# Optimization experiments

Hardware: AMD Instinct MI355X
Metric: run time of the kernel (lower is better)

The kernel has to match this reference:

```python
import jax, jax.numpy as jnp
import numpy as np

L, B, N, C, H = 6, 4, 512, 512, 8
D = C // H          # head_dim = 64
MLP = 4 * C         # mlp_ratio = 4.0
EPS = 1e-6


def setup_inputs() -> dict:
    key = jax.random.key(0)
    ks = jax.random.split(key, 12)
    p = lambda k, sh: jax.random.normal(k, sh, dtype=jnp.float32) * 0.02
    return {
        "x": jax.random.normal(ks[0], (B, N, C), dtype=jnp.float32),
        "time_emb": jax.random.normal(ks[1], (B, C), dtype=jnp.float32),
        "pair_emb": jax.random.normal(ks[2], (B, H, N, N), dtype=jnp.float32) * 0.1,
        "is_padded_mask": jnp.zeros((B, 1, 1, N), dtype=bool),
        # per-block stacked params (leading dim = L blocks)
        "wq": p(ks[3], (L, C, C)),
        "wk": p(ks[4], (L, C, C)),
        "wv": p(ks[5], (L, C, C)),
        "wo": p(ks[6], (L, C, C)),
        "bo": jnp.zeros((L, C), dtype=jnp.float32),
        "w1": p(ks[7], (L, C, MLP)),
        "b1": jnp.zeros((L, MLP), dtype=jnp.float32),
        "w2": p(ks[8], (L, MLP, C)),
        "b2": jnp.zeros((L, C), dtype=jnp.float32),
        "wada": p(ks[9], (L, C, 6 * C)),
        "bada": jnp.zeros((L, 6 * C), dtype=jnp.float32),
    }


def _ln(x):
    # LayerNorm without affine, eps=1e-6 (torch elementwise_affine=False)
    mu = jnp.mean(x, axis=-1, keepdims=True)
    var = jnp.mean(jnp.square(x - mu), axis=-1, keepdims=True)
    return (x - mu) * jax.lax.rsqrt(var + EPS)


def _modulate(x, shift, scale):
    return x * (1.0 + scale[:, None, :]) + shift[:, None, :]


def reference(x, time_emb, pair_emb, is_padded_mask,
              wq, wk, wv, wo, bo, w1, b1, w2, b2, wada, bada):
    scale = D ** -0.5
    t_act = jax.nn.silu(time_emb)  # shared SiLU input to adaLN of each block
    for i in range(L):
        ada = t_act @ wada[i] + bada[i]  # (B, 6C)
        sh_msa, sc_msa, g_msa, sh_mlp, sc_mlp, g_mlp = jnp.split(ada, 6, axis=1)
        # fill_attn_mask: masked_fill padded key positions with -inf
        pair = jnp.where(is_padded_mask, -jnp.inf, pair_emb)  # (B,H,N,N)
        mx = _modulate(_ln(x), sh_msa, sc_msa)  # (B,N,C)
        q = (mx @ wq[i]).reshape(B, N, H, D)
        k = (mx @ wk[i]).reshape(B, N, H, D)
        v = (mx @ wv[i]).reshape(B, N, H, D)
        qk = jnp.einsum('bnhd,bshd->bhns', q, k) * scale  # (B,H,N,N)
        attn = jax.nn.softmax(qk + pair, axis=-1)
        o = jnp.einsum('bhns,bshd->bnhd', attn, v).reshape(B, N, C)
        o = o @ wo[i] + bo[i]
        x = x + g_msa[:, None, :] * o
        pair_emb = pair + qk  # residual on pair embedding
        h = _modulate(_ln(x), sh_mlp, sc_mlp)
        h = jax.nn.gelu(h @ w1[i] + b1[i], approximate=True) @ w2[i] + b2[i]
        x = x + g_mlp[:, None, :] * h
    return x, pair_emb
```

## Files before the change

kernel.cpp:

```cpp
#include <hip/hip_runtime.h>
#include <hip/hip_bf16.h>

#define LNUM 6
#define BB 4
#define NSEQ 512
#define CDIM 512
#define HNUM 8
#define DHEAD 64
#define MLPD 2048
#define MROWS (BB*NSEQ)

typedef __hip_bfloat16 bf16;
typedef __attribute__((ext_vector_type(4))) float f32x4;
typedef __attribute__((ext_vector_type(8))) short bf16x8;

__device__ __forceinline__ void gld_lds16(const bf16* g, bf16* l) {
  __builtin_amdgcn_global_load_lds((const __attribute__((address_space(1))) void*)g,
                                   (__attribute__((address_space(3))) void*)l, 16, 0, 0);
}

__device__ __forceinline__ float gelu_tanh(float t) {
  float u = 0.7978845608028654f * (t + 0.044715f * t * t * t);
  u = fminf(fmaxf(u, -15.f), 15.f);
  float e = __expf(2.f * u);
  return 0.5f * t * (1.f + (e - 1.f) / (e + 1.f));
}

enum { EP_BF16 = 0, EP_RESID = 2, EP_GELU = 3, EP_QKV = 4 };

template<int BM, int BN, int MODE>
__global__ __launch_bounds__(256) void gemm_nt(
    const bf16* __restrict__ A, int lda,
    const bf16* __restrict__ Bt, int ldb,
    int K, int zdiv,
    long sA1, long sA2, long sB1, long sB2, long sO1, long sO2,
    bf16* __restrict__ obf, int ldo,
    const float* __restrict__ bias,
    const float* __restrict__ ada, int gate_off,
    float* __restrict__ xres,
    bf16* __restrict__ vtout)
{
  constexpr int FM = BM / 32, FN = BN / 32;
  __shared__ bf16 lA[2 * BM * 64];
  __shared__ bf16 lB[2 * BN * 64];
  const int tid = threadIdx.x;
  const int wid = tid >> 6, lane = tid & 63;
  const int z = blockIdx.z;
  const long z1 = z / zdiv, z2 = z % zdiv;
  A  += z1 * sA1 + z2 * sA2;
  Bt += z1 * sB1 + z2 * sB2;
  const long obase = z1 * sO1 + z2 * sO2;
  const int m0 = blockIdx.x * BM;
  const int n0 = blockIdx.y * BN;
  const int wm = wid >> 1, wn = wid & 1;
  const int srow = tid >> 3, scl = tid & 7;

  f32x4 zero = {0.f, 0.f, 0.f, 0.f};
  f32x4 acc[FM][FN];
#pragma unroll
  for (int i = 0; i < FM; i++)
#pragma unroll
    for (int j = 0; j < FN; j++) acc[i][j] = zero;

  auto stage = [&](int buf, int kt) {
#pragma unroll
    for (int p = 0; p < BM / 32; p++) {
      const int rr = (p << 5) + srow;
      const int gk = (scl ^ (rr & 7)) << 3;
      gld_lds16(A + (size_t)(m0 + rr) * lda + (kt << 6) + gk,
                lA + buf * (BM * 64) + (p << 11) + (wid << 9));
    }
#pragma unroll
    for (int p = 0; p < BN / 32; p++) {
      const int rr = (p << 5) + srow;
      const int gk = (scl ^ (rr & 7)) << 3;
      gld_lds16(Bt + (size_t)(n0 + rr) * ldb + (kt << 6) + gk,
                lB + buf * (BN * 64) + (p << 11) + (wid << 9));
    }
  };

  const int rlo = lane & 15, kq = lane >> 4;
  auto compute = [&](int buf) {
#pragma unroll
    for (int kk = 0; kk < 2; kk++) {
      bf16x8 af[FM], bg[FN];
#pragma unroll
      for (int i = 0; i < FM; i++) {
        const int ra = wm * (BM / 2) + (i << 4) + rlo;
        af[i] = *(const bf16x8*)(lA + buf * (BM * 64) + (ra << 6) +
                                 ((((kk << 2) + kq) ^ (ra & 7)) << 3));
      }
#pragma unroll
      for (int j = 0; j < FN; j++) {
        const int rb2 = wn * (BN / 2) + (j << 4) + rlo;
        bg[j] = *(const bf16x8*)(lB + buf * (BN * 64) + (rb2 << 6) +
                                 ((((kk << 2) + kq) ^ (rb2 & 7)) << 3));
      }
#pragma unroll
      for (int i = 0; i < FM; i++)
#pragma unroll
        for (int j = 0; j < FN; j++)
          acc[i][j] = __builtin_amdgcn_mfma_f32_16x16x32_bf16(af[i], bg[j], acc[i][j], 0, 0, 0);
    }
  };

  const int NT = K >> 6;
  stage(0, 0);
  for (int t = 0; t < NT - 1; t++) {
    stage((t + 1) & 1, t + 1);
    if constexpr ((BM + BN) / 32 == 4)      asm volatile("s_waitcnt vmcnt(4)" ::: "memory");
    else if constexpr ((BM + BN) / 32 == 6) asm volatile("s_waitcnt vmcnt(6)" ::: "memory");
    else                                    asm volatile("s_waitcnt vmcnt(8)" ::: "memory");
    __builtin_amdgcn_s_barrier();
    asm volatile("" ::: "memory");
    compute(t & 1);
    asm volatile("" ::: "memory");
    __builtin_amdgcn_s_barrier();
  }
  asm volatile("s_waitcnt vmcnt(0)" ::: "memory");
  __builtin_amdgcn_s_barrier();
  asm volatile("" ::: "memory");
  compute((NT - 1) & 1);

  const int cl = lane & 15, rb = (lane >> 4) << 2;
#pragma unroll
  for (int i = 0; i < FM; i++) {
#pragma unroll
    for (int j = 0; j < FN; j++) {
      const int gc = n0 + wn * (BN / 2) + (j << 4) + cl;
#pragma unroll
      for (int r = 0; r < 4; r++) {
        const int gr = m0 + wm * (BM / 2) + (i << 4) + rb + r;
        float v = acc[i][j][r];
        if (MODE == EP_BF16) {
          obf[obase + (size_t)gr * ldo + gc] = __float2bfloat16(v);
        } else if (MODE == EP_QKV) {
          if (gc < 2 * CDIM) {
            obf[obase + (size_t)gr * ldo + gc] = __float2bfloat16(v);
          } else {
            const int b = gr >> 9, n = gr & 511, hd = gc - 2 * CDIM;
            vtout[((size_t)((b << 3) + (hd >> 6)) * 64 + (hd & 63)) * 512 + n] = __float2bfloat16(v);
          }
        } else if (MODE == EP_RESID) {
          const int b = gr >> 9;
          float t2 = v + bias[gc];
          xres[(size_t)gr * CDIM + gc] += ada[b * (6 * CDIM) + gate_off + gc] * t2;
        } else {
          float t2 = v + bias[gc];
          obf[obase + (size_t)gr * ldo + gc] = __float2bfloat16(gelu_tanh(t2));
        }
      }
    }
  }
}

__global__ __launch_bounds__(256) void attn_fused(
    const bf16* __restrict__ qkv, const bf16* __restrict__ vt,
    const float* __restrict__ pair_in, float* __restrict__ pair_out,
    const unsigned char* __restrict__ mask,
    bf16* __restrict__ obuf, float scale)
{
  __shared__ bf16 lQ[64 * 64];
  __shared__ bf16 lK[2][64 * 64];
  __shared__ bf16 lV[2][64 * 64];
  __shared__ bf16 lP[64 * 64];
  const int tid = threadIdx.x, wid = tid >> 6;
  const int lane = tid & 63;
  const int z = blockIdx.z, b = z >> 3, h = z & 7;
  const int m0 = blockIdx.x * 64;
  const int srow = tid >> 3, scl = tid & 7;
  const bf16* Aq = qkv + (size_t)b * NSEQ * 1536 + h * 64;
  const bf16* Bk = Aq + CDIM;
  const bf16* Bv = vt + (size_t)z * DHEAD * NSEQ;
  const size_t pz = (size_t)z * NSEQ * NSEQ;
  const int rlo = lane & 15, kq = lane >> 4, cl = rlo;

#pragma unroll
  for (int r = 0; r < 2; r++) {
    const int rr = (r << 5) + srow;
    const int gk = (scl ^ (rr & 7)) << 3;
    gld_lds16(Aq + (size_t)(m0 + rr) * 1536 + gk, lQ + (r << 11) + (wid << 9));
    gld_lds16(Bk + (size_t)rr * 1536 + gk, lK[0] + (r << 11) + (wid << 9));
    gld_lds16(Bv + (size_t)rr * NSEQ + gk, lV[0] + (r << 11) + (wid << 9));
  }

  float m_run[4], l_run[4];
  f32x4 oacc[4];
  f32x4 zero = {0.f, 0.f, 0.f, 0.f};
#pragma unroll
  for (int r = 0; r < 4; r++) { m_run[r] = -INFINITY; l_run[r] = 0.f; }
#pragma unroll
  for (int j = 0; j < 4; j++) oacc[j] = zero;
  bf16x8 afq[2];

  float prA[4][4]; bool mkA[4];
  float prB[4][4]; bool mkB[4];
#pragma unroll
  for (int j = 0; j < 4; j++) {
#pragma unroll
    for (int r = 0; r < 4; r++)
      prA[j][r] = pair_in[pz + (size_t)(m0 + (wid << 4) + (kq << 2) + r) * NSEQ + ((j << 4) + cl)];
    mkA[j] = mask[b * NSEQ + (j << 4) + cl] != 0;
  }

  for (int ct = 0; ct < 8; ct++) {
    const int cur = ct & 1;
    asm volatile("s_waitcnt vmcnt(0)" ::: "memory");
    __builtin_amdgcn_s_barrier();
    asm volatile("" ::: "memory");

    if (ct == 0) {
#pragma unroll
      for (int kk = 0; kk < 2; kk++) {
        const int ra = (wid << 4) + rlo;
        afq[kk] = *(const bf16x8*)(lQ + (ra << 6) + ((((kk << 2) + kq) ^ (ra & 7)) << 3));
      }
    }

    if (ct < 7) {
#pragma unroll
      for (int r = 0; r < 2; r++) {
        const int rr = (r << 5) + srow;
        const int gk = (scl ^ (rr & 7)) << 3;
        gld_lds16(Bk + (size_t)((ct + 1) * 64 + rr) * 1536 + gk,
                  lK[cur ^ 1] + (r << 11) + (wid << 9));
        gld_lds16(Bv + (size_t)rr * NSEQ + (ct + 1) * 64 + gk,
                  lV[cur ^ 1] + (r << 11) + (wid << 9));
      }
#pragma unroll
      for (int j = 0; j < 4; j++) {
#pragma unroll
        for (int r = 0; r < 4; r++)
          prB[j][r] = pair_in[pz + (size_t)(m0 + (wid << 4) + (kq << 2) + r) * NSEQ +
                              ((ct + 1) * 64 + (j << 4) + cl)];
        mkB[j] = mask[b * NSEQ + (ct + 1) * 64 + (j << 4) + cl] != 0;
      }
    }

    f32x4 s[4];
#pragma unroll
    for (int j = 0; j < 4; j++) s[j] = zero;
#pragma unroll
    for (int kk = 0; kk < 2; kk++)
#pragma unroll
      for (int j = 0; j < 4; j++) {
        const int rk = (j << 4) + rlo;
        bf16x8 bk = *(const bf16x8*)(lK[cur] + (rk << 6) + ((((kk << 2) + kq) ^ (rk & 7)) << 3));
        s[j] = __builtin_amdgcn_mfma_f32_16x16x32_bf16(afq[kk], bk, s[j], 0, 0, 0);
      }

    float p[4][4];
#pragma unroll
    for (int r = 0; r < 4; r++) {
      const size_t prow = pz + (size_t)(m0 + (wid << 4) + (kq << 2) + r) * NSEQ + ct * 64;
      float sf[4];
#pragma unroll
      for (int j = 0; j < 4; j++) {
        float pp = mkA[j] ? -INFINITY : prA[j][r];
        sf[j] = s[j][r] * scale + pp;
        pair_out[prow + (j << 4) + cl] = sf[j];
      }
      float tm = fmaxf(fmaxf(sf[0], sf[1]), fmaxf(sf[2], sf[3]));
#pragma unroll
      for (int o = 1; o < 16; o <<= 1) tm = fmaxf(tm, __shfl_xor(tm, o));
      const float mnew = fmaxf(m_run[r], tm);
      const float fr = __expf(m_run[r] - mnew);
      float rs = 0.f;
#pragma unroll
      for (int j = 0; j < 4; j++) { p[j][r] = __expf(sf[j] - mnew); rs += p[j][r]; }
#pragma unroll
      for (int o = 1; o < 16; o <<= 1) rs += __shfl_xor(rs, o);
      l_run[r] = l_run[r] * fr + rs;
      m_run[r] = mnew;
#pragma unroll
      for (int j = 0; j < 4; j++) oacc[j][r] *= fr;
    }

#pragma unroll
    for (int j = 0; j < 4; j++)
#pragma unroll
      for (int r = 0; r < 4; r++) {
        const int row = (wid << 4) + (kq << 2) + r;
        const int col = (j << 4) + cl;
        lP[(row << 6) + (((col >> 3) ^ (row & 7)) << 3) + (col & 7)] = __float2bfloat16(p[j][r]);
      }
    asm volatile("s_waitcnt lgkmcnt(0)" ::: "memory");
    __builtin_amdgcn_sched_barrier(0);

#pragma unroll
    for (int kk = 0; kk < 2; kk++) {
      const int ra = (wid << 4) + rlo;
      bf16x8 ap = *(const bf16x8*)(lP + (ra << 6) + ((((kk << 2) + kq) ^ (ra & 7)) << 3));
#pragma unroll
      for (int j = 0; j < 4; j++) {
        const int rd = (j << 4) + rlo;
        bf16x8 bv = *(const bf16x8*)(lV[cur] + (rd << 6) + ((((kk << 2) + kq) ^ (rd & 7)) << 3));
        oacc[j] = __builtin_amdgcn_mfma_f32_16x16x32_bf16(ap, bv, oacc[j], 0, 0, 0);
      }
    }

    if (ct < 7) {
#pragma unroll
      for (int j = 0; j < 4; j++) {
#pragma unroll
        for (int r = 0; r < 4; r++) prA[j][r] = prB[j][r];
        mkA[j] = mkB[j];
      }
    }
  }

#pragma unroll
  for (int j = 0; j < 4; j++)
#pragma unroll
    for (int r = 0; r < 4; r++) {
      const int gr = m0 + (wid << 4) + (kq << 2) + r;
      const int gc = h * 64 + (j << 4) + cl;
      obuf[((size_t)b * NSEQ + gr) * CDIM + gc] = __float2bfloat16(oacc[j][r] / l_run[r]);
    }
}

__global__ __launch_bounds__(256) void ln_mod(const float* __restrict__ x,
                                              const float* __restrict__ ada,
                                              int sh_off, int sc_off,
                                              bf16* __restrict__ out)
{
  const int row = blockIdx.x;
  const int b = row >> 9;
  const float* xr = x + (size_t)row * CDIM;
  const int t = threadIdx.x;
  float2 v = ((const float2*)xr)[t];
  float s = v.x + v.y;
  float ss = v.x * v.x + v.y * v.y;
#pragma unroll
  for (int o = 32; o > 0; o >>= 1) { s += __shfl_down(s, o); ss += __shfl_down(ss, o); }
  __shared__ float red[8];
  __shared__ float mv[2];
  const int w = t >> 6, ln = t & 63;
  if (ln == 0) { red[w] = s; red[4 + w] = ss; }
  __syncthreads();
  if (t == 0) {
    float S = red[0] + red[1] + red[2] + red[3];
    float SS = red[4] + red[5] + red[6] + red[7];
    float mu = S * (1.0f / CDIM);
    float var = SS * (1.0f / CDIM) - mu * mu;
    mv[0] = mu; mv[1] = rsqrtf(var + 1e-6f);
  }
  __syncthreads();
  const float mu = mv[0], rs = mv[1];
  const float* adab = ada + b * (6 * CDIM);
  const int c = t * 2;
  float o0 = (v.x - mu) * rs * (1.0f + adab[sc_off + c])     + adab[sh_off + c];
  float o1 = (v.y - mu) * rs * (1.0f + adab[sc_off + c + 1]) + adab[sh_off + c + 1];
  out[(size_t)row * CDIM + c]     = __float2bfloat16(o0);
  out[(size_t)row * CDIM + c + 1] = __float2bfloat16(o1);
}

__global__ __launch_bounds__(256) void ada_part(const float* __restrict__ te,
                                                const float* __restrict__ wada,
                                                float* __restrict__ partial)
{
  __shared__ float ta[4][64];
  const int layer = blockIdx.z, kc = blockIdx.y;
  const int t = threadIdx.x;
  {
    const int b = t >> 6, kk = t & 63;
    float xx = te[b * CDIM + kc * 64 + kk];
    ta[b][kk] = xx / (1.f + __expf(-xx));
  }
  __syncthreads();
  const int col = blockIdx.x * 512 + t * 2;
  const float* W = wada + ((size_t)layer * CDIM + kc * 64) * 3072 + col;
  float2 acc0 = {0, 0}, acc1 = {0, 0}, acc2 = {0, 0}, acc3 = {0, 0};
#pragma unroll 8
  for (int kk = 0; kk < 64; kk++) {
    float2 w = *(const float2*)(W + (size_t)kk * 3072);
    acc0.x = fmaf(ta[0][kk], w.x, acc0.x); acc0.y = fmaf(ta[0][kk], w.y, acc0.y);
    acc1.x = fmaf(ta[1][kk], w.x, acc1.x); acc1.y = fmaf(ta[1][kk], w.y, acc1.y);
    acc2.x = fmaf(ta[2][kk], w.x, acc2.x); acc2.y = fmaf(ta[2][kk], w.y, acc2.y);
    acc3.x = fmaf(ta[3][kk], w.x, acc3.x); acc3.y = fmaf(ta[3][kk], w.y, acc3.y);
  }
  float* pp = partial + (((size_t)(layer * 8 + kc) * 4) * 3072);
  *(float2*)(pp + 0 * 3072 + col) = acc0;
  *(float2*)(pp + 1 * 3072 + col) = acc1;
  *(float2*)(pp + 2 * 3072 + col) = acc2;
  *(float2*)(pp + 3 * 3072 + col) = acc3;
}

__global__ __launch_bounds__(256) void ada_reduce(const float* __restrict__ partial,
                                                  const float* __restrict__ bada,
                                                  float* __restrict__ adab)
{
  const int idx = blockIdx.x * 256 + threadIdx.x;
  const int layer = idx / 12288, rem = idx % 12288;
  const int b = rem / 3072, col = rem % 3072;
  float acc = bada[layer * 3072 + col];
#pragma unroll
  for (int kc = 0; kc < 8; kc++)
    acc += partial[((size_t)(layer * 8 + kc) * 4 + b) * 3072 + col];
  adab[((size_t)layer * 4 + b) * 3072 + col] = acc;
}

__global__ __launch_bounds__(256) void conv_t(const float* __restrict__ src, bf16* __restrict__ dst,
                                              int R, int Ccols, long sS, long sD)
{
  src += (size_t)blockIdx.z * sS;
  dst += (size_t)blockIdx.z * sD;
  __shared__ float tb[32][33];
  const int c0 = blockIdx.x * 32, r0 = blockIdx.y * 32;
  const int tx = threadIdx.x & 31, ty = threadIdx.x >> 5;
#pragma unroll
  for (int i = ty; i < 32; i += 8) tb[i][tx] = src[(size_t)(r0 + i) * Ccols + c0 + tx];
  __syncthreads();
#pragma unroll
  for (int i = ty; i < 32; i += 8) dst[(size_t)(c0 + i) * R + r0 + tx] = __float2bfloat16(tb[tx][i]);
}

extern "C" void kernel_launch(void* const* d_in, const int* in_sizes, int n_in,
                              void* d_out, int out_size, void* d_ws, size_t ws_size,
                              hipStream_t stream)
{
  (void)in_sizes; (void)n_in; (void)out_size; (void)ws_size;
  const float* in_x    = (const float*)d_in[0];
  const float* in_te   = (const float*)d_in[1];
  const float* in_pair = (const float*)d_in[2];
  const unsigned char* in_mask = (const unsigned char*)d_in[3];
  const float* wq   = (const float*)d_in[4];
  const float* wk   = (const float*)d_in[5];
  const float* wv   = (const float*)d_in[6];
  const float* wo   = (const float*)d_in[7];
  const float* bo   = (const float*)d_in[8];
  const float* w1   = (const float*)d_in[9];
  const float* b1   = (const float*)d_in[10];
  const float* w2   = (const float*)d_in[11];
  const float* b2   = (const float*)d_in[12];
  const float* wada = (const float*)d_in[13];
  const float* bada = (const float*)d_in[14];

  float* xout = (float*)d_out;
  float* pairout = xout + (size_t)BB * NSEQ * CDIM;

  char* ws = (char*)d_ws;
  size_t off = 0;
  auto alloc = [&](size_t bytes) -> void* {
    void* p = ws + off; off += (bytes + 255) & ~(size_t)255; return p;
  };
  bf16*  wqkvT = (bf16*)alloc((size_t)LNUM * 1536 * 512 * 2);
  bf16*  woT   = (bf16*)alloc((size_t)LNUM * 512 * 512 * 2);
  bf16*  w1T   = (bf16*)alloc((size_t)LNUM * 2048 * 512 * 2);
  bf16*  w2T   = (bf16*)alloc((size_t)LNUM * 512 * 2048 * 2);
  float* adab  = (float*)alloc((size_t)LNUM * BB * 6 * CDIM * 4);
  float* apart = (float*)alloc((size_t)LNUM * 8 * BB * 3072 * 4);
  bf16*  mx    = (bf16*)alloc((size_t)MROWS * CDIM * 2);
  bf16*  qkv   = (bf16*)alloc((size_t)MROWS * 1536 * 2);
  bf16*  vt    = (bf16*)alloc((size_t)BB * HNUM * DHEAD * NSEQ * 2);
  bf16*  obuf  = (bf16*)alloc((size_t)MROWS * CDIM * 2);
  bf16*  hbuf  = (bf16*)alloc((size_t)MROWS * MLPD * 2);

  hipMemcpyAsync(xout, in_x, (size_t)MROWS * CDIM * 4, hipMemcpyDeviceToDevice, stream);

  conv_t<<<dim3(16, 16, LNUM), 256, 0, stream>>>(wq, wqkvT,               512, 512,  (long)512 * 512,  (long)1536 * 512);
  conv_t<<<dim3(16, 16, LNUM), 256, 0, stream>>>(wk, wqkvT + 512 * 512,   512, 512,  (long)512 * 512,  (long)1536 * 512);
  conv_t<<<dim3(16, 16, LNUM), 256, 0, stream>>>(wv, wqkvT + 2 * 512 * 512, 512, 512, (long)512 * 512, (long)1536 * 512);
  conv_t<<<dim3(16, 16, LNUM), 256, 0, stream>>>(wo, woT,                 512, 512,  (long)512 * 512,  (long)512 * 512);
  conv_t<<<dim3(64, 16, LNUM), 256, 0, stream>>>(w1, w1T,                 512, 2048, (long)512 * 2048, (long)2048 * 512);
  conv_t<<<dim3(16, 64, LNUM), 256, 0, stream>>>(w2, w2T,                 2048, 512, (long)2048 * 512, (long)512 * 2048);

  ada_part<<<dim3(6, 8, LNUM), 256, 0, stream>>>(in_te, wada, apart);
  ada_reduce<<<dim3(LNUM * BB * 3072 / 256), 256, 0, stream>>>(apart, bada, adab);

  const float scale = 0.125f;
  for (int i = 0; i < LNUM; i++) {
    const float* adal = adab + (size_t)i * BB * 6 * CDIM;
    ln_mod<<<MROWS, 256, 0, stream>>>(xout, adal, 0, CDIM, mx);
    gemm_nt<128, 64, EP_QKV><<<dim3(16, 24, 1), 256, 0, stream>>>(
        mx, CDIM, wqkvT + (size_t)i * 1536 * 512, CDIM, CDIM, 1,
        0, 0, 0, 0, 0, 0,
        qkv, 1536, nullptr, nullptr, 0, nullptr, vt);
    const float* pin = (i == 0) ? in_pair : pairout;
    attn_fused<<<dim3(8, 1, 32), 256, 0, stream>>>(qkv, vt, pin, pairout, in_mask, obuf, scale);
    gemm_nt<64, 64, EP_RESID><<<dim3(32, 8, 1), 256, 0, stream>>>(
        obuf, CDIM, woT + (size_t)i * CDIM * CDIM, CDIM, CDIM, 1,
        0, 0, 0, 0, 0, 0,
        nullptr, CDIM, bo + (size_t)i * CDIM, adal, 2 * CDIM, xout, nullptr);
    ln_mod<<<MROWS, 256, 0, stream>>>(xout, adal, 3 * CDIM, 4 * CDIM, mx);
    gemm_nt<128, 128, EP_GELU><<<dim3(16, 16, 1), 256, 0, stream>>>(
        mx, CDIM, w1T + (size_t)i * MLPD * CDIM, CDIM, CDIM, 1,
        0, 0, 0, 0, 0, 0,
        hbuf, MLPD, b1 + (size_t)i * MLPD, nullptr, 0, nullptr, nullptr);
    gemm_nt<64, 64, EP_RESID><<<dim3(32, 8, 1), 256, 0, stream>>>(
        hbuf, MLPD, w2T + (size_t)i * CDIM * MLPD, MLPD, MLPD, 1,
        0, 0, 0, 0, 0, 0,
        nullptr, CDIM, b2 + (size_t)i * CDIM, adal, 5 * CDIM, xout, nullptr);
  }
}
```

Before: 592.1 us.

## Shrink GEMM tiles, split V transpose into its own kernel, drop pair prefetch

All GEMMs move to smaller tiles (64x64 for QKV and MLP1, 32x64 for the residual GEMMs), which launches more blocks on the many CUs and adds a vmcnt(3) case for the new tile shape. The V-transpose scatter is taken out of the QKV epilogue and done by a separate LDS-tiled transpose kernel, so the GEMM epilogue stores are uniform. The attention kernel no longer double-buffers pair/mask values in registers and loads them for the current tile instead, which cuts register pressure but exposes that load latency. The costs are an extra launch and more operand re-reads from the smaller tiles.

Result: faster. 530.0 us (-10.5%).

```diff
diff --git a/kernel.cpp b/kernel.cpp
--- a/kernel.cpp
+++ b/kernel.cpp
@@ -26,7 +26,7 @@
   return 0.5f * t * (1.f + (e - 1.f) / (e + 1.f));
 }
 
-enum { EP_BF16 = 0, EP_RESID = 2, EP_GELU = 3, EP_QKV = 4 };
+enum { EP_BF16 = 0, EP_RESID = 2, EP_GELU = 3 };
 
 template<int BM, int BN, int MODE>
 __global__ __launch_bounds__(256) void gemm_nt(
@@ -37,8 +37,7 @@
     bf16* __restrict__ obf, int ldo,
     const float* __restrict__ bias,
     const float* __restrict__ ada, int gate_off,
-    float* __restrict__ xres,
-    bf16* __restrict__ vtout)
+    float* __restrict__ xres)
 {
   constexpr int FM = BM / 32, FN = BN / 32;
   __shared__ bf16 lA[2 * BM * 64];
@@ -108,9 +107,11 @@
   stage(0, 0);
   for (int t = 0; t < NT - 1; t++) {
     stage((t + 1) & 1, t + 1);
-    if constexpr ((BM + BN) / 32 == 4)      asm volatile("s_waitcnt vmcnt(4)" ::: "memory");
-    else if constexpr ((BM + BN) / 32 == 6) asm volatile("s_waitcnt vmcnt(6)" ::: "memory");
-    else                                    asm volatile("s_waitcnt vmcnt(8)" ::: "memory");
+    constexpr int NL = (BM + BN) / 32;
+    if constexpr (NL == 3)      asm volatile("s_waitcnt vmcnt(3)" ::: "memory");
+    else if constexpr (NL == 4) asm volatile("s_waitcnt vmcnt(4)" ::: "memory");
+    else if constexpr (NL == 6) asm volatile("s_waitcnt vmcnt(6)" ::: "memory");
+    else                        asm volatile("s_waitcnt vmcnt(8)" ::: "memory");
     __builtin_amdgcn_s_barrier();
     asm volatile("" ::: "memory");
     compute(t & 1);
@@ -134,13 +135,6 @@
         float v = acc[i][j][r];
         if (MODE == EP_BF16) {
           obf[obase + (size_t)gr * ldo + gc] = __float2bfloat16(v);
-        } else if (MODE == EP_QKV) {
-          if (gc < 2 * CDIM) {
-            obf[obase + (size_t)gr * ldo + gc] = __float2bfloat16(v);
-          } else {
-            const int b = gr >> 9, n = gr & 511, hd = gc - 2 * CDIM;
-            vtout[((size_t)((b << 3) + (hd >> 6)) * 64 + (hd & 63)) * 512 + n] = __float2bfloat16(v);
-          }
         } else if (MODE == EP_RESID) {
           const int b = gr >> 9;
           float t2 = v + bias[gc];
@@ -164,8 +158,7 @@
   __shared__ bf16 lK[2][64 * 64];
   __shared__ bf16 lV[2][64 * 64];
   __shared__ bf16 lP[64 * 64];
-  const int tid = threadIdx.x, wid = tid >> 6;
-  const int lane = tid & 63;
+  const int tid = threadIdx.x, wid = tid >> 6, lane = tid & 63;
   const int z = blockIdx.z, b = z >> 3, h = z & 7;
   const int m0 = blockIdx.x * 64;
   const int srow = tid >> 3, scl = tid & 7;
@@ -193,16 +186,6 @@
   for (int j = 0; j < 4; j++) oacc[j] = zero;
   bf16x8 afq[2];
 
-  float prA[4][4]; bool mkA[4];
-  float prB[4][4]; bool mkB[4];
-#pragma unroll
-  for (int j = 0; j < 4; j++) {
-#pragma unroll
-    for (int r = 0; r < 4; r++)
-      prA[j][r] = pair_in[pz + (size_t)(m0 + (wid << 4) + (kq << 2) + r) * NSEQ + ((j << 4) + cl)];
-    mkA[j] = mask[b * NSEQ + (j << 4) + cl] != 0;
-  }
-
   for (int ct = 0; ct < 8; ct++) {
     const int cur = ct & 1;
     asm volatile("s_waitcnt vmcnt(0)" ::: "memory");
@@ -227,15 +210,19 @@
         gld_lds16(Bv + (size_t)rr * NSEQ + (ct + 1) * 64 + gk,
                   lV[cur ^ 1] + (r << 11) + (wid << 9));
       }
-#pragma unroll
-      for (int j = 0; j < 4; j++) {
-#pragma unroll
-        for (int r = 0; r < 4; r++)
-          prB[j][r] = pair_in[pz + (size_t)(m0 + (wid << 4) + (kq << 2) + r) * NSEQ +
-                              ((ct + 1) * 64 + (j << 4) + cl)];
-        mkB[j] = mask[b * NSEQ + (ct + 1) * 64 + (j << 4) + cl] != 0;
-      }
-    }
+    }
+
+    float pr[4][4];
+#pragma unroll
+    for (int j = 0; j < 4; j++)
+#pragma unroll
+      for (int r = 0; r < 4; r++)
+        pr[j][r] = pair_in[pz + (size_t)(m0 + (wid << 4) + (kq << 2) + r) * NSEQ +
+                           (ct * 64 + (j << 4) + cl)];
+    bool mk[4];
+#pragma unroll
+    for (int j = 0; j < 4; j++)
+      mk[j] = mask[b * NSEQ + ct * 64 + (j << 4) + cl] != 0;
 
     f32x4 s[4];
 #pragma unroll
@@ -256,7 +243,7 @@
       float sf[4];
 #pragma unroll
       for (int j = 0; j < 4; j++) {
-        float pp = mkA[j] ? -INFINITY : prA[j][r];
+        float pp = mk[j] ? -INFINITY : pr[j][r];
         sf[j] = s[j][r] * scale + pp;
         pair_out[prow + (j << 4) + cl] = sf[j];
       }
@@ -296,15 +283,6 @@
         const int rd = (j << 4) + rlo;
         bf16x8 bv = *(const bf16x8*)(lV[cur] + (rd << 6) + ((((kk << 2) + kq) ^ (rd & 7)) << 3));
         oacc[j] = __builtin_amdgcn_mfma_f32_16x16x32_bf16(ap, bv, oacc[j], 0, 0, 0);
-      }
-    }
-
-    if (ct < 7) {
-#pragma unroll
-      for (int j = 0; j < 4; j++) {
-#pragma unroll
-        for (int r = 0; r < 4; r++) prA[j][r] = prB[j][r];
-        mkA[j] = mkB[j];
       }
     }
   }
@@ -413,6 +391,21 @@
   __syncthreads();
 #pragma unroll
   for (int i = ty; i < 32; i += 8) dst[(size_t)(c0 + i) * R + r0 + tx] = __float2bfloat16(tb[tx][i]);
+}
+
+__global__ __launch_bounds__(256) void vtrans(const bf16* __restrict__ qkv, bf16* __restrict__ vt)
+{
+  const int z = blockIdx.z, b = z >> 3, h = z & 7;
+  const bf16* src = qkv + (size_t)b * NSEQ * 1536 + 2 * CDIM + h * DHEAD;
+  bf16* dst = vt + (size_t)z * DHEAD * NSEQ;
+  __shared__ bf16 tb[32][33];
+  const int n0 = blockIdx.x * 32, d0 = blockIdx.y * 32;
+  const int tx = threadIdx.x & 31, ty = threadIdx.x >> 5;
+#pragma unroll
+  for (int i = ty; i < 32; i += 8) tb[i][tx] = src[(size_t)(n0 + i) * 1536 + d0 + tx];
+  __syncthreads();
+#pragma unroll
+  for (int i = ty; i < 32; i += 8) dst[(size_t)(d0 + i) * NSEQ + n0 + tx] = tb[tx][i];
 }
 
 extern "C" void kernel_launch(void* const* d_in, const int* in_sizes, int n_in,
@@ -472,24 +465,25 @@
   for (int i = 0; i < LNUM; i++) {
     const float* adal = adab + (size_t)i * BB * 6 * CDIM;
     ln_mod<<<MROWS, 256, 0, stream>>>(xout, adal, 0, CDIM, mx);
-    gemm_nt<128, 64, EP_QKV><<<dim3(16, 24, 1), 256, 0, stream>>>(
+    gemm_nt<64, 64, EP_BF16><<<dim3(32, 24, 1), 256, 0, stream>>>(
         mx, CDIM, wqkvT + (size_t)i * 1536 * 512, CDIM, CDIM, 1,
         0, 0, 0, 0, 0, 0,
-        qkv, 1536, nullptr, nullptr, 0, nullptr, vt);
+        qkv, 1536, nullptr, nullptr, 0, nullptr);
+    vtrans<<<dim3(16, 2, 32), 256, 0, stream>>>(qkv, vt);
     const float* pin = (i == 0) ? in_pair : pairout;
     attn_fused<<<dim3(8, 1, 32), 256, 0, stream>>>(qkv, vt, pin, pairout, in_mask, obuf, scale);
-    gemm_nt<64, 64, EP_RESID><<<dim3(32, 8, 1), 256, 0, stream>>>(
+    gemm_nt<32, 64, EP_RESID><<<dim3(64, 8, 1), 256, 0, stream>>>(
         obuf, CDIM, woT + (size_t)i * CDIM * CDIM, CDIM, CDIM, 1,
         0, 0, 0, 0, 0, 0,
-        nullptr, CDIM, bo + (size_t)i * CDIM, adal, 2 * CDIM, xout, nullptr);
+        nullptr, CDIM, bo + (size_t)i * CDIM, adal, 2 * CDIM, xout);
     ln_mod<<<MROWS, 256, 0, stream>>>(xout, adal, 3 * CDIM, 4 * CDIM, mx);
-    gemm_nt<128, 128, EP_GELU><<<dim3(16, 16, 1), 256, 0, stream>>>(
+    gemm_nt<64, 64, EP_GELU><<<dim3(32, 32, 1), 256, 0, stream>>>(
         mx, CDIM, w1T + (size_t)i * MLPD * CDIM, CDIM, CDIM, 1,
         0, 0, 0, 0, 0, 0,
-        hbuf, MLPD, b1 + (size_t)i * MLPD, nullptr, 0, nullptr, nullptr);
-    gemm_nt<64, 64, EP_RESID><<<dim3(32, 8, 1), 256, 0, stream>>>(
+        hbuf, MLPD, b1 + (size_t)i * MLPD, nullptr, 0, nullptr);
+    gemm_nt<32, 64, EP_RESID><<<dim3(64, 8, 1), 256, 0, stream>>>(
         hbuf, MLPD, w2T + (size_t)i * CDIM * MLPD, MLPD, MLPD, 1,
         0, 0, 0, 0, 0, 0,
-        nullptr, CDIM, b2 + (size_t)i * CDIM, adal, 5 * CDIM, xout, nullptr);
-  }
-}
+        nullptr, CDIM, b2 + (size_t)i * CDIM, adal, 5 * CDIM, xout);
+  }
+}
```
